# Performance work log

Hardware: AMD Instinct MI355X
Metric: run time of the kernel (lower is better)

## Reference

```python
import jax, jax.numpy as jnp
import numpy as np

L, P, R, A, V, B = 2, 3, 512, 196, 9487, 256


def setup_inputs() -> dict:
    key = jax.random.key(0)
    ks = jax.random.split(key, 20)
    s = 0.02
    inp = {
        "x": jax.random.normal(ks[0], (B, R), jnp.float32),
        "att": jax.random.normal(ks[1], (B, A, R), jnp.float32),
        "inputs": jax.random.normal(ks[2], (2 * L, B, R), jnp.float32),
        # per-layer, per-parallel LSTM core weights (torch Linear: y = x W^T + b)
        "i2h_w": s * jax.random.normal(ks[3], (L, P, 4 * R, R), jnp.float32),
        "i2h_b": s * jax.random.normal(ks[4], (L, P, 4 * R), jnp.float32),
        "h2h_w": s * jax.random.normal(ks[5], (L, P, 4 * R, R), jnp.float32),
        "h2h_b": s * jax.random.normal(ks[6], (L, P, 4 * R), jnp.float32),
        "a2h_w": s * jax.random.normal(ks[7], (L, P, 4 * R, R), jnp.float32),
        "a2h_b": s * jax.random.normal(ks[8], (L, P, 4 * R), jnp.float32),
        # 2 attention modules per layer
        "a2a_w": s * jax.random.normal(ks[9], (L, 2, A, R), jnp.float32),
        "a2a_b": s * jax.random.normal(ks[10], (L, 2, A), jnp.float32),
        "h2a_w": s * jax.random.normal(ks[11], (L, 2, A, R), jnp.float32),
        "h2a_b": s * jax.random.normal(ks[12], (L, 2, A), jnp.float32),
        "d2d_w": s * jax.random.normal(ks[13], (L, 2, A), jnp.float32),
        "d2d_b": s * jax.random.normal(ks[14], (L, 2), jnp.float32),
        "proj_w": s * jax.random.normal(ks[15], (V, R), jnp.float32),
        "proj_b": s * jax.random.normal(ks[16], (V,), jnp.float32),
    }
    return inp


def _soft_att(att, h, a2a_w, a2a_b, h2a_w, h2a_b, d2d_w, d2d_b):
    # att: [B,A,R], h: [B,R]
    v = jnp.einsum('bar,kr->bak', att, a2a_w) + a2a_b          # [B,A,A]
    hh = h @ h2a_w.T + h2a_b                                   # [B,A]
    dot = jnp.tanh(v + hh[:, :, None])                         # [B,A,A]
    score = jnp.einsum('bak,k->ba', dot, d2d_w) + d2d_b        # [B,A]
    w = jax.nn.softmax(score, axis=-1)
    return jnp.einsum('bar,ba->br', att, w)                    # [B,R]


def reference(x, att, inputs, i2h_w, i2h_b, h2h_w, h2h_b, a2h_w, a2h_b,
              a2a_w, a2a_b, h2a_w, h2a_b, d2d_w, d2d_b, proj_w, proj_b):
    outputs = []
    top_h = None
    for i in range(L):
        prev_c = inputs[2 * i]
        prev_h = inputs[2 * i + 1]
        xt = x if i == 0 else x + outputs[-1]
        att_res0 = _soft_att(att, prev_h, a2a_w[i, 0], a2a_b[i, 0],
                             h2a_w[i, 0], h2a_b[i, 0], d2d_w[i, 0], d2d_b[i, 0])
        # fused gates over the P parallel cores: [P,B,4R]
        sums = (jnp.einsum('bi,pgi->pbg', xt, i2h_w[i]) + i2h_b[i][:, None, :]
                + jnp.einsum('bi,pgi->pbg', prev_h, h2h_w[i]) + h2h_b[i][:, None, :]
                + jnp.einsum('bi,pgi->pbg', att_res0, a2h_w[i]) + a2h_b[i][:, None, :])
        sig = jax.nn.sigmoid(sums[..., :3 * R])
        in_g, fg_g, out_g = sig[..., :R], sig[..., R:2 * R], sig[..., 2 * R:3 * R]
        in_t = jnp.tanh(sums[..., 3 * R:])
        nc_p = fg_g * prev_c + in_g * in_t                     # [P,B,R]
        nh_p = out_g * jnp.tanh(nc_p)                          # [P,B,R]
        next_c = nc_p.mean(0)
        next_h = nh_p.mean(0)
        att_res1 = _soft_att(att, next_h, a2a_w[i, 1], a2a_b[i, 1],
                             h2a_w[i, 1], h2a_b[i, 1], d2d_w[i, 1], d2d_b[i, 1])
        top_h = att_res1 + next_h
        outputs.append(next_c)
        outputs.append(top_h)
    logsoft = jax.nn.log_softmax(top_h @ proj_w.T + proj_b, axis=-1)
    return jnp.stack(outputs), logsoft
```

## Files before the change

### kernel.cpp

```cpp
#include <hip/hip_runtime.h>
#include <hip/hip_bf16.h>
#include <math.h>

#define L_ 2
#define P_ 3
#define R_ 512
#define A_ 196
#define V_ 9487
#define B_ 256
#define BR (B_*R_)
#define G4 (4*R_)

typedef short bf16x8 __attribute__((ext_vector_type(8)));
typedef float f32x4  __attribute__((ext_vector_type(4)));

static __device__ __forceinline__ unsigned short f2b(float f){
  unsigned int u = __builtin_bit_cast(unsigned int, f);
  u += 0x7fffu + ((u >> 16) & 1u);
  return (unsigned short)(u >> 16);
}
static __device__ __forceinline__ bf16x8 cvt8(float4 a, float4 b){
  bf16x8 r;
  r[0]=(short)f2b(a.x); r[1]=(short)f2b(a.y); r[2]=(short)f2b(a.z); r[3]=(short)f2b(a.w);
  r[4]=(short)f2b(b.x); r[5]=(short)f2b(b.y); r[6]=(short)f2b(b.z); r[7]=(short)f2b(b.w);
  return r;
}

__global__ __launch_bounds__(256) void k_cvt(const float* __restrict__ src,
                                             short* __restrict__ dst, int n)
{
  const int c = blockIdx.x * 256 + threadIdx.x;
  const int base = c * 8;
  if (base >= n) return;
  float4 a = *(const float4*)(src + base);
  float4 b = *(const float4*)(src + base + 4);
  *(bf16x8*)(dst + base) = cvt8(a, b);
}

__global__ __launch_bounds__(256) void k_hh(
    const float* __restrict__ h, const float* __restrict__ hw,
    const float* __restrict__ hb, float* __restrict__ out)
{
  __shared__ float hred[64][5];
  const int t = threadIdx.x;
  const int row = blockIdx.x * 64 + (t >> 2);
  const int seg = t & 3;
  const int b = row / A_;
  const int a = row - b * A_;
  const float* hp = h  + (size_t)b * R_ + seg * 128;
  const float* wp = hw + (size_t)a * R_ + seg * 128;
  float p = 0.f;
#pragma unroll
  for (int k = 0; k < 128; k += 4) {
    float4 a4 = *(const float4*)(hp + k);
    float4 b4 = *(const float4*)(wp + k);
    p = fmaf(a4.x, b4.x, p); p = fmaf(a4.y, b4.y, p);
    p = fmaf(a4.z, b4.z, p); p = fmaf(a4.w, b4.w, p);
  }
  hred[t >> 2][seg] = p;
  __syncthreads();
  if (t < 64) {
    const int m = blockIdx.x * 64 + t;
    const int b2 = m / A_;
    const int a2 = m - b2 * A_;
    out[m] = hred[t][0] + hred[t][1] + hred[t][2] + hred[t][3] + hb[a2];
  }
}

__global__ __launch_bounds__(256) void k_score_mfma(
    const float* __restrict__ att, const short* __restrict__ wbf,
    const float* __restrict__ a2ab, const float* __restrict__ d2dw,
    const float* __restrict__ d2db, const float* __restrict__ hh,
    float* __restrict__ score)
{
  __shared__ __align__(16) short As[4 * 64 * 8];
  __shared__ __align__(16) short Bs[4 * 224 * 8];
  __shared__ float wpad[224], bpad[224], hhs[64], sred[2][64];

  const int t   = threadIdx.x;
  const int m0  = blockIdx.x * 64;
  const int wid = t >> 6, l = t & 63;
  const int wr  = wid >> 1, wc = wid & 1;
  const int q   = l >> 4, lc = l & 15;

  if (t < 224) { wpad[t] = (t < A_) ? d2dw[t] : 0.f; bpad[t] = (t < A_) ? a2ab[t] : 0.f; }
  if (t < 64)  hhs[t] = hh[m0 + t];

  f32x4 acc[2][7];
#pragma unroll
  for (int i = 0; i < 2; ++i)
#pragma unroll
    for (int j = 0; j < 7; ++j) acc[i][j] = (f32x4){0.f, 0.f, 0.f, 0.f};

  const int s_row = t >> 2, s_kb = t & 3;
  const float* asrc = att + (size_t)(m0 + s_row) * R_ + s_kb * 8;
  const int n3 = 192 + s_row;

  float4 ra0, ra1;
  bf16x8 rb0, rb1, rb2, rb3;

#define SC_LOAD(ks) {                                                   \
    const int k0 = (ks) * 32;                                           \
    ra0 = *(const float4*)(asrc + k0);                                  \
    ra1 = *(const float4*)(asrc + k0 + 4);                              \
    const int koff = k0 + s_kb * 8;                                     \
    rb0 = *(const bf16x8*)(wbf + (size_t)(s_row      ) * R_ + koff);    \
    rb1 = *(const bf16x8*)(wbf + (size_t)(s_row +  64) * R_ + koff);    \
    rb2 = *(const bf16x8*)(wbf + (size_t)(s_row + 128) * R_ + koff);    \
    if (t < 128) {                                                      \
      if (n3 < A_) rb3 = *(const bf16x8*)(wbf + (size_t)n3 * R_ + koff);\
      else         rb3 = (bf16x8){0,0,0,0,0,0,0,0};                     \
    }                                                                   \
  }
#define SC_STORE() {                                                    \
    *(bf16x8*)&As[s_kb * 512  + s_row * 8] = cvt8(ra0, ra1);            \
    *(bf16x8*)&Bs[s_kb * 1792 + (s_row      ) * 8] = rb0;               \
    *(bf16x8*)&Bs[s_kb * 1792 + (s_row +  64) * 8] = rb1;               \
    *(bf16x8*)&Bs[s_kb * 1792 + (s_row + 128) * 8] = rb2;               \
    if (t < 128) *(bf16x8*)&Bs[s_kb * 1792 + n3 * 8] = rb3;             \
  }

  SC_LOAD(0);
  for (int ks = 0; ks < 16; ++ks) {
    __syncthreads();
    SC_STORE();
    __syncthreads();
    if (ks < 15) SC_LOAD(ks + 1);
    bf16x8 af[2], bfr[7];
#pragma unroll
    for (int mf = 0; mf < 2; ++mf) {
      const int row = wr * 32 + mf * 16 + lc;
      af[mf] = *(const bf16x8*)&As[q * 512 + row * 8];
    }
#pragma unroll
    for (int nf = 0; nf < 7; ++nf) {
      const int n = wc * 112 + nf * 16 + lc;
      bfr[nf] = *(const bf16x8*)&Bs[q * 1792 + n * 8];
    }
#pragma unroll
    for (int mf = 0; mf < 2; ++mf)
#pragma unroll
      for (int nf = 0; nf < 7; ++nf)
        acc[mf][nf] = __builtin_amdgcn_mfma_f32_16x16x32_bf16(af[mf], bfr[nf], acc[mf][nf], 0, 0, 0);
  }
#undef SC_LOAD
#undef SC_STORE

  float s[2][4];
#pragma unroll
  for (int mf = 0; mf < 2; ++mf)
#pragma unroll
    for (int r = 0; r < 4; ++r) s[mf][r] = 0.f;

#pragma unroll
  for (int mf = 0; mf < 2; ++mf) {
    const int rbase = wr * 32 + mf * 16 + q * 4;
#pragma unroll
    for (int nf = 0; nf < 7; ++nf) {
      const int col = wc * 112 + nf * 16 + lc;
      const float bp = bpad[col], wp = wpad[col];
#pragma unroll
      for (int r = 0; r < 4; ++r)
        s[mf][r] += tanhf(acc[mf][nf][r] + bp + hhs[rbase + r]) * wp;
    }
  }
#pragma unroll
  for (int mask = 1; mask <= 8; mask <<= 1) {
#pragma unroll
    for (int mf = 0; mf < 2; ++mf)
#pragma unroll
      for (int r = 0; r < 4; ++r) s[mf][r] += __shfl_xor(s[mf][r], mask);
  }
  if (lc == 0) {
#pragma unroll
    for (int mf = 0; mf < 2; ++mf)
#pragma unroll
      for (int r = 0; r < 4; ++r)
        sred[wc][wr * 32 + mf * 16 + q * 4 + r] = s[mf][r];
  }
  __syncthreads();
  if (t < 64) score[m0 + t] = sred[0][t] + sred[1][t] + d2db[0];
}

__global__ __launch_bounds__(256) void k_softmax_att(float* __restrict__ sc)
{
  __shared__ float red[256];
  const int b = blockIdx.x, t = threadIdx.x;
  float v = (t < A_) ? sc[b*A_ + t] : -INFINITY;
  red[t] = v; __syncthreads();
  for (int s = 128; s > 0; s >>= 1) { if (t < s) red[t] = fmaxf(red[t], red[t+s]); __syncthreads(); }
  const float mx = red[0]; __syncthreads();
  const float e = (t < A_) ? expf(v - mx) : 0.f;
  red[t] = e; __syncthreads();
  for (int s = 128; s > 0; s >>= 1) { if (t < s) red[t] += red[t+s]; __syncthreads(); }
  if (t < A_) sc[b*A_ + t] = e / red[0];
}

__global__ __launch_bounds__(256) void k_attres(
    const float* __restrict__ att, const float* __restrict__ w, float* __restrict__ out)
{
  __shared__ float wl[A_];
  const int b = blockIdx.x, t = threadIdx.x;
  if (t < A_) wl[t] = w[b*A_ + t];
  __syncthreads();
  const int r = blockIdx.y * 256 + t;
  const float* ap = att + (size_t)b * A_ * R_ + r;
  float acc = 0.f;
#pragma unroll 4
  for (int a = 0; a < A_; ++a) acc = fmaf(ap[(size_t)a * R_], wl[a], acc);
  out[b * R_ + r] = acc;
}

__global__ __launch_bounds__(256) void k_lstm_mfma(
    const float* __restrict__ xt, const float* __restrict__ ph, const float* __restrict__ ar,
    const short* __restrict__ wi, const short* __restrict__ wh, const short* __restrict__ wa,
    int layer, float* __restrict__ sums)
{
  __shared__ __align__(16) short As[4 * 64 * 8];
  __shared__ __align__(16) short Bs[4 * 128 * 8];

  const int t   = threadIdx.x;
  const int m0  = blockIdx.x * 64;
  const int n0  = blockIdx.y * 128;
  const int wid = t >> 6, l = t & 63;
  const int wr  = wid >> 1, wc = wid & 1;
  const int q   = l >> 4, lc = l & 15;

  f32x4 acc[2][4];
#pragma unroll
  for (int i = 0; i < 2; ++i)
#pragma unroll
    for (int j = 0; j < 4; ++j) acc[i][j] = (f32x4){0.f, 0.f, 0.f, 0.f};

  const int s_row = t >> 2, s_kb = t & 3;
  const size_t wrow0 = ((size_t)layer * 6144 + n0) * R_;

  float4 ra0, ra1;
  bf16x8 rb0, rb1;

#define LS_LOAD(ks) {                                                   \
    const int seg = (ks) >> 4;                                          \
    const int kk  = ((ks) & 15) * 32;                                   \
    const float* asel = (seg == 0) ? xt : (seg == 1) ? ph : ar;         \
    const float* ap = asel + (size_t)(m0 + s_row) * R_ + kk + s_kb * 8; \
    ra0 = *(const float4*)ap;                                           \
    ra1 = *(const float4*)(ap + 4);                                     \
    const short* wsel = (seg == 0) ? wi : (seg == 1) ? wh : wa;         \
    const short* bp0 = wsel + wrow0 + (size_t)(s_row      ) * R_ + kk + s_kb * 8; \
    const short* bp1 = wsel + wrow0 + (size_t)(s_row +  64) * R_ + kk + s_kb * 8; \
    rb0 = *(const bf16x8*)bp0;                                          \
    rb1 = *(const bf16x8*)bp1;                                          \
  }
#define LS_STORE() {                                                    \
    *(bf16x8*)&As[s_kb * 512  + s_row * 8] = cvt8(ra0, ra1);            \
    *(bf16x8*)&Bs[s_kb * 1024 + (s_row      ) * 8] = rb0;               \
    *(bf16x8*)&Bs[s_kb * 1024 + (s_row + 64) * 8] = rb1;                \
  }

  LS_LOAD(0);
  for (int ks = 0; ks < 48; ++ks) {
    __syncthreads();
    LS_STORE();
    __syncthreads();
    if (ks < 47) LS_LOAD(ks + 1);
    bf16x8 af[2], bfr[4];
#pragma unroll
    for (int mf = 0; mf < 2; ++mf) {
      const int row = wr * 32 + mf * 16 + lc;
      af[mf] = *(const bf16x8*)&As[q * 512 + row * 8];
    }
#pragma unroll
    for (int nf = 0; nf < 4; ++nf) {
      const int n = wc * 64 + nf * 16 + lc;
      bfr[nf] = *(const bf16x8*)&Bs[q * 1024 + n * 8];
    }
#pragma unroll
    for (int mf = 0; mf < 2; ++mf)
#pragma unroll
      for (int nf = 0; nf < 4; ++nf)
        acc[mf][nf] = __builtin_amdgcn_mfma_f32_16x16x32_bf16(af[mf], bfr[nf], acc[mf][nf], 0, 0, 0);
  }
#undef LS_LOAD
#undef LS_STORE

#pragma unroll
  for (int mf = 0; mf < 2; ++mf) {
#pragma unroll
    for (int nf = 0; nf < 4; ++nf) {
      const int col = n0 + wc * 64 + nf * 16 + lc;
      const int p = col >> 11, g = col & 2047;
#pragma unroll
      for (int r = 0; r < 4; ++r) {
        const int b = m0 + wr * 32 + mf * 16 + q * 4 + r;
        sums[((size_t)p * B_ + b) * (size_t)G4 + g] = acc[mf][nf][r];
      }
    }
  }
}

__global__ __launch_bounds__(256) void k_lstm_elem(
    const float* __restrict__ sums,
    const float* __restrict__ i2hb, const float* __restrict__ h2hb, const float* __restrict__ a2hb,
    const float* __restrict__ prev_c, int layer,
    float* __restrict__ out_c, float* __restrict__ next_h)
{
  const int idx = blockIdx.x * 256 + threadIdx.x;
  const int b = idx >> 9, r = idx & 511;
  const size_t boff = (size_t)layer * P_ * G4;
  const float pc = prev_c[idx];
  float aC = 0.f, aH = 0.f;
#pragma unroll
  for (int p = 0; p < P_; ++p) {
    const float* sp = sums + ((size_t)p * B_ + b) * (size_t)G4;
    const float* b1 = i2hb + boff + p * G4;
    const float* b2 = h2hb + boff + p * G4;
    const float* b3 = a2hb + boff + p * G4;
    const float gi = sp[r]      + b1[r]      + b2[r]      + b3[r];
    const float gf = sp[r+512]  + b1[r+512]  + b2[r+512]  + b3[r+512];
    const float go = sp[r+1024] + b1[r+1024] + b2[r+1024] + b3[r+1024];
    const float gt = sp[r+1536] + b1[r+1536] + b2[r+1536] + b3[r+1536];
    const float ig = 1.f / (1.f + expf(-gi));
    const float fg = 1.f / (1.f + expf(-gf));
    const float og = 1.f / (1.f + expf(-go));
    const float it = tanhf(gt);
    const float nc = fg * pc + ig * it;
    const float nh = og * tanhf(nc);
    aC += nc; aH += nh;
  }
  out_c[idx]  = aC * (1.f/3.f);
  next_h[idx] = aH * (1.f/3.f);
}

__global__ __launch_bounds__(256) void k_toph(
    const float* __restrict__ attres, const float* __restrict__ nh, const float* __restrict__ x,
    float* __restrict__ out_slot, float* __restrict__ toph, float* __restrict__ xt_next, int make_xt)
{
  const int idx = blockIdx.x * 256 + threadIdx.x;
  const float v = attres[idx] + nh[idx];
  out_slot[idx] = v;
  toph[idx] = v;
  if (make_xt) xt_next[idx] = x[idx] + v;
}

__global__ __launch_bounds__(256) void k_proj_mfma(
    const float* __restrict__ th, const short* __restrict__ pwb,
    const float* __restrict__ pb, float* __restrict__ logits)
{
  __shared__ __align__(16) short As[4 * 64 * 8];
  __shared__ __align__(16) short Bs[4 * 128 * 8];

  const int t   = threadIdx.x;
  const int m0  = blockIdx.x * 64;
  const int n0  = blockIdx.y * 128;
  const int wid = t >> 6, l = t & 63;
  const int wr  = wid >> 1, wc = wid & 1;
  const int q   = l >> 4, lc = l & 15;

  f32x4 acc[2][4];
#pragma unroll
  for (int i = 0; i < 2; ++i)
#pragma unroll
    for (int j = 0; j < 4; ++j) acc[i][j] = (f32x4){0.f, 0.f, 0.f, 0.f};

  const int s_row = t >> 2, s_kb = t & 3;
  const int ng0 = n0 + s_row, ng1 = n0 + s_row + 64;

  float4 ra0, ra1;
  bf16x8 rb0, rb1;

#define PJ_LOAD(ks) {                                                   \
    const int kk = (ks) * 32;                                           \
    const float* ap = th + (size_t)(m0 + s_row) * R_ + kk + s_kb * 8;   \
    ra0 = *(const float4*)ap;                                           \
    ra1 = *(const float4*)(ap + 4);                                     \
    if (ng0 < V_) rb0 = *(const bf16x8*)(pwb + (size_t)ng0 * R_ + kk + s_kb * 8); \
    else          rb0 = (bf16x8){0,0,0,0,0,0,0,0};                      \
    if (ng1 < V_) rb1 = *(const bf16x8*)(pwb + (size_t)ng1 * R_ + kk + s_kb * 8); \
    else          rb1 = (bf16x8){0,0,0,0,0,0,0,0};                      \
  }
#define PJ_STORE() {                                                    \
    *(bf16x8*)&As[s_kb * 512  + s_row * 8] = cvt8(ra0, ra1);            \
    *(bf16x8*)&Bs[s_kb * 1024 + (s_row      ) * 8] = rb0;               \
    *(bf16x8*)&Bs[s_kb * 1024 + (s_row + 64) * 8] = rb1;                \
  }

  PJ_LOAD(0);
  for (int ks = 0; ks < 16; ++ks) {
    __syncthreads();
    PJ_STORE();
    __syncthreads();
    if (ks < 15) PJ_LOAD(ks + 1);
    bf16x8 af[2], bfr[4];
#pragma unroll
    for (int mf = 0; mf < 2; ++mf) {
      const int row = wr * 32 + mf * 16 + lc;
      af[mf] = *(const bf16x8*)&As[q * 512 + row * 8];
    }
#pragma unroll
    for (int nf = 0; nf < 4; ++nf) {
      const int n = wc * 64 + nf * 16 + lc;
      bfr[nf] = *(const bf16x8*)&Bs[q * 1024 + n * 8];
    }
#pragma unroll
    for (int mf = 0; mf < 2; ++mf)
#pragma unroll
      for (int nf = 0; nf < 4; ++nf)
        acc[mf][nf] = __builtin_amdgcn_mfma_f32_16x16x32_bf16(af[mf], bfr[nf], acc[mf][nf], 0, 0, 0);
  }
#undef PJ_LOAD
#undef PJ_STORE

#pragma unroll
  for (int mf = 0; mf < 2; ++mf) {
#pragma unroll
    for (int nf = 0; nf < 4; ++nf) {
      const int col = n0 + wc * 64 + nf * 16 + lc;
      if (col < V_) {
        const float bias = pb[col];
#pragma unroll
        for (int r = 0; r < 4; ++r) {
          const int b = m0 + wr * 32 + mf * 16 + q * 4 + r;
          logits[(size_t)b * V_ + col] = acc[mf][nf][r] + bias;
        }
      }
    }
  }
}

__global__ __launch_bounds__(256) void k_logsoftmax(
    const float* __restrict__ logits, float* __restrict__ out)
{
  __shared__ float red[256];
  const int b = blockIdx.x, t = threadIdx.x;
  const float* lp = logits + (size_t)b * V_;
  float mx = -INFINITY;
  for (int n = t; n < V_; n += 256) mx = fmaxf(mx, lp[n]);
  red[t] = mx; __syncthreads();
  for (int s = 128; s > 0; s >>= 1) { if (t < s) red[t] = fmaxf(red[t], red[t+s]); __syncthreads(); }
  mx = red[0]; __syncthreads();
  float sm = 0.f;
  for (int n = t; n < V_; n += 256) sm += expf(lp[n] - mx);
  red[t] = sm; __syncthreads();
  for (int s = 128; s > 0; s >>= 1) { if (t < s) red[t] += red[t+s]; __syncthreads(); }
  const float lse = mx + logf(red[0]);
  float* op = out + (size_t)b * V_;
  for (int n = t; n < V_; n += 256) op[n] = lp[n] - lse;
}

extern "C" void kernel_launch(void* const* d_in, const int* in_sizes, int n_in,
                              void* d_out, int out_size, void* d_ws, size_t ws_size,
                              hipStream_t stream)
{
  const float* x      = (const float*)d_in[0];
  const float* att    = (const float*)d_in[1];
  const float* inputs = (const float*)d_in[2];
  const float* i2hw   = (const float*)d_in[3];
  const float* i2hb   = (const float*)d_in[4];
  const float* h2hw   = (const float*)d_in[5];
  const float* h2hb   = (const float*)d_in[6];
  const float* a2hw   = (const float*)d_in[7];
  const float* a2hb   = (const float*)d_in[8];
  const float* a2aw   = (const float*)d_in[9];
  const float* a2ab   = (const float*)d_in[10];
  const float* h2aw   = (const float*)d_in[11];
  const float* h2ab   = (const float*)d_in[12];
  const float* d2dw   = (const float*)d_in[13];
  const float* d2db   = (const float*)d_in[14];
  const float* pw     = (const float*)d_in[15];
  const float* pb     = (const float*)d_in[16];
  float* out = (float*)d_out;
  float* ws  = (float*)d_ws;

  float* w_score  = ws + 0;
  float* w_hh     = ws + 51200;
  float* w_attres = ws + 102400;
  float* w_xt     = ws + 233472;
  float* w_nexth  = ws + 364544;
  float* w_toph   = ws + 495616;
  float* w_sums   = ws + 626688;
  float* w_logits = ws + 2199552;

  short* bfbase = (short*)(ws + 4628480);
  short* aw_bf  = bfbase;
  short* wi_bf  = bfbase + 401408;
  short* wh_bf  = bfbase + 6692864;
  short* wa_bf  = bfbase + 12984320;
  short* pw_bf  = bfbase + 19275776;

  k_cvt<<<196,  256, 0, stream>>>(a2aw, aw_bf, 401408);
  k_cvt<<<3072, 256, 0, stream>>>(i2hw, wi_bf, 6291456);
  k_cvt<<<3072, 256, 0, stream>>>(h2hw, wh_bf, 6291456);
  k_cvt<<<3072, 256, 0, stream>>>(a2hw, wa_bf, 6291456);
  k_cvt<<<2372, 256, 0, stream>>>(pw,   pw_bf, 4857344);

  const float* cur_x = x;
  for (int i = 0; i < L_; ++i) {
    const float* prev_c = inputs + (size_t)(2*i)   * BR;
    const float* prev_h = inputs + (size_t)(2*i+1) * BR;

    {
      const int idx = i*2 + 0;
      k_hh<<<784, 256, 0, stream>>>(prev_h, h2aw + (size_t)idx*A_*R_, h2ab + (size_t)idx*A_, w_hh);
      k_score_mfma<<<784, 256, 0, stream>>>(att, aw_bf + (size_t)idx*A_*R_,
          a2ab + (size_t)idx*A_, d2dw + (size_t)idx*A_, d2db + idx, w_hh, w_score);
      k_softmax_att<<<B_, 256, 0, stream>>>(w_score);
      k_attres<<<dim3(B_, 2), 256, 0, stream>>>(att, w_score, w_attres);
    }

    k_lstm_mfma<<<dim3(4, 48), 256, 0, stream>>>(cur_x, prev_h, w_attres,
                                                 wi_bf, wh_bf, wa_bf, i, w_sums);
    k_lstm_elem<<<512, 256, 0, stream>>>(w_sums, i2hb, h2hb, a2hb, prev_c, i,
                                         out + (size_t)(2*i) * BR, w_nexth);

    {
      const int idx = i*2 + 1;
      k_hh<<<784, 256, 0, stream>>>(w_nexth, h2aw + (size_t)idx*A_*R_, h2ab + (size_t)idx*A_, w_hh);
      k_score_mfma<<<784, 256, 0, stream>>>(att, aw_bf + (size_t)idx*A_*R_,
          a2ab + (size_t)idx*A_, d2dw + (size_t)idx*A_, d2db + idx, w_hh, w_score);
      k_softmax_att<<<B_, 256, 0, stream>>>(w_score);
      k_attres<<<dim3(B_, 2), 256, 0, stream>>>(att, w_score, w_attres);
    }

    k_toph<<<512, 256, 0, stream>>>(w_attres, w_nexth, x,
                                    out + (size_t)(2*i+1) * BR, w_toph, w_xt,
                                    (i == 0) ? 1 : 0);
    cur_x = w_xt;
  }

  k_proj_mfma<<<dim3(4, 75), 256, 0, stream>>>(w_toph, pw_bf, pb, w_logits);
  k_logsoftmax<<<B_, 256, 0, stream>>>(w_logits, out + (size_t)4 * BR);
}
```

Measured before the change: 752.0 us.

## Convert att to bf16 once, use async LDS loads and fuse softmax with attres

Adds a one-time pass that converts the whole att tensor to bf16 and pads the a2a weights to 256 rows. The score GEMM then loads tiles straight into LDS with global_load_lds, using a swizzled, double-buffered layout, instead of converting float att inside each tile. Softmax and the attention-weighted sum are merged into one kernel that reads bf16 att, which halves the bytes read per attention pass. The cost is an extra conversion pass over the 25.7M-element att tensor (read 103MB fp32, write 51MB bf16) and lower precision in attres.

```diff
diff --git a/kernel.cpp b/kernel.cpp
--- a/kernel.cpp
+++ b/kernel.cpp
@@ -13,11 +13,16 @@
 
 typedef short bf16x8 __attribute__((ext_vector_type(8)));
 typedef float f32x4  __attribute__((ext_vector_type(4)));
+typedef unsigned int u32;
 
 static __device__ __forceinline__ unsigned short f2b(float f){
-  unsigned int u = __builtin_bit_cast(unsigned int, f);
+  u32 u = __builtin_bit_cast(u32, f);
   u += 0x7fffu + ((u >> 16) & 1u);
   return (unsigned short)(u >> 16);
+}
+static __device__ __forceinline__ float b2f(short s){
+  u32 u = ((u32)(unsigned short)s) << 16;
+  return __builtin_bit_cast(float, u);
 }
 static __device__ __forceinline__ bf16x8 cvt8(float4 a, float4 b){
   bf16x8 r;
@@ -25,6 +30,14 @@
   r[4]=(short)f2b(b.x); r[5]=(short)f2b(b.y); r[6]=(short)f2b(b.z); r[7]=(short)f2b(b.w);
   return r;
 }
+
+static __device__ __forceinline__ void gld16(const void* g, void* l){
+  __builtin_amdgcn_global_load_lds(
+      (const __attribute__((address_space(1))) u32*)g,
+      (__attribute__((address_space(3))) u32*)l, 16, 0, 0);
+}
+
+#define SW(x) ((((x)&3) ^ (((x)>>2)&3)))
 
 __global__ __launch_bounds__(256) void k_cvt(const float* __restrict__ src,
                                              short* __restrict__ dst, int n)
@@ -35,6 +48,24 @@
   float4 a = *(const float4*)(src + base);
   float4 b = *(const float4*)(src + base + 4);
   *(bf16x8*)(dst + base) = cvt8(a, b);
+}
+
+__global__ __launch_bounds__(256) void k_cvt_pad_aw(const float* __restrict__ src,
+                                                    short* __restrict__ dst)
+{
+  const int idx8 = (blockIdx.x * 256 + threadIdx.x) * 8;
+  const int g   = idx8 >> 17;
+  const int rem = idx8 & 131071;
+  const int row = rem >> 9;
+  const int k   = rem & 511;
+  bf16x8 v;
+  if (row < A_) {
+    const float* sp = src + ((size_t)g * A_ + row) * R_ + k;
+    v = cvt8(*(const float4*)sp, *(const float4*)(sp + 4));
+  } else {
+    v = (bf16x8){0,0,0,0,0,0,0,0};
+  }
+  *(bf16x8*)(dst + idx8) = v;
 }
 
 __global__ __launch_bounds__(256) void k_hh(
@@ -68,14 +99,14 @@
 }
 
 __global__ __launch_bounds__(256) void k_score_mfma(
-    const float* __restrict__ att, const short* __restrict__ wbf,
+    const short* __restrict__ att_bf, const short* __restrict__ wbf,
     const float* __restrict__ a2ab, const float* __restrict__ d2dw,
     const float* __restrict__ d2db, const float* __restrict__ hh,
     float* __restrict__ score)
 {
-  __shared__ __align__(16) short As[4 * 64 * 8];
-  __shared__ __align__(16) short Bs[4 * 224 * 8];
-  __shared__ float wpad[224], bpad[224], hhs[64], sred[2][64];
+  __shared__ __align__(16) short As[2][256 * 8];
+  __shared__ __align__(16) short Bs[2][1024 * 8];
+  __shared__ float wpad[256], bpad[256], hhs[64], sred[2][64];
 
   const int t   = threadIdx.x;
   const int m0  = blockIdx.x * 64;
@@ -83,68 +114,59 @@
   const int wr  = wid >> 1, wc = wid & 1;
   const int q   = l >> 4, lc = l & 15;
 
-  if (t < 224) { wpad[t] = (t < A_) ? d2dw[t] : 0.f; bpad[t] = (t < A_) ? a2ab[t] : 0.f; }
-  if (t < 64)  hhs[t] = hh[m0 + t];
-
-  f32x4 acc[2][7];
+  wpad[t] = (t < A_) ? d2dw[t] : 0.f;
+  bpad[t] = (t < A_) ? a2ab[t] : 0.f;
+  if (t < 64) hhs[t] = hh[m0 + t];
+
+  f32x4 acc[2][8];
 #pragma unroll
   for (int i = 0; i < 2; ++i)
 #pragma unroll
-    for (int j = 0; j < 7; ++j) acc[i][j] = (f32x4){0.f, 0.f, 0.f, 0.f};
-
-  const int s_row = t >> 2, s_kb = t & 3;
-  const float* asrc = att + (size_t)(m0 + s_row) * R_ + s_kb * 8;
-  const int n3 = 192 + s_row;
-
-  float4 ra0, ra1;
-  bf16x8 rb0, rb1, rb2, rb3;
-
-#define SC_LOAD(ks) {                                                   \
-    const int k0 = (ks) * 32;                                           \
-    ra0 = *(const float4*)(asrc + k0);                                  \
-    ra1 = *(const float4*)(asrc + k0 + 4);                              \
-    const int koff = k0 + s_kb * 8;                                     \
-    rb0 = *(const bf16x8*)(wbf + (size_t)(s_row      ) * R_ + koff);    \
-    rb1 = *(const bf16x8*)(wbf + (size_t)(s_row +  64) * R_ + koff);    \
-    rb2 = *(const bf16x8*)(wbf + (size_t)(s_row + 128) * R_ + koff);    \
-    if (t < 128) {                                                      \
-      if (n3 < A_) rb3 = *(const bf16x8*)(wbf + (size_t)n3 * R_ + koff);\
-      else         rb3 = (bf16x8){0,0,0,0,0,0,0,0};                     \
-    }                                                                   \
-  }
-#define SC_STORE() {                                                    \
-    *(bf16x8*)&As[s_kb * 512  + s_row * 8] = cvt8(ra0, ra1);            \
-    *(bf16x8*)&Bs[s_kb * 1792 + (s_row      ) * 8] = rb0;               \
-    *(bf16x8*)&Bs[s_kb * 1792 + (s_row +  64) * 8] = rb1;               \
-    *(bf16x8*)&Bs[s_kb * 1792 + (s_row + 128) * 8] = rb2;               \
-    if (t < 128) *(bf16x8*)&Bs[s_kb * 1792 + n3 * 8] = rb3;             \
-  }
-
-  SC_LOAD(0);
+    for (int j = 0; j < 8; ++j) acc[i][j] = (f32x4){0.f, 0.f, 0.f, 0.f};
+
+  const int a_row  = t >> 2;
+  const int a_kb   = (t & 3) ^ SW(a_row);
+  const short* a_g = att_bf + (size_t)(m0 + a_row) * R_ + a_kb * 8;
+  int b_n[4], b_kb[4];
+#pragma unroll
+  for (int j = 0; j < 4; ++j) {
+    b_n[j]  = j * 64 + (t >> 2);
+    b_kb[j] = (t & 3) ^ SW(b_n[j]);
+  }
+
+#define STAGE(bufi, kz) {                                                 \
+    gld16((const void*)(a_g + (kz)), (void*)&As[bufi][wid * 512]);        \
+    _Pragma("unroll")                                                     \
+    for (int j = 0; j < 4; ++j)                                           \
+      gld16((const void*)(wbf + (size_t)b_n[j] * R_ + (kz) + b_kb[j] * 8),\
+            (void*)&Bs[bufi][j * 2048 + wid * 512]);                      \
+  }
+
+  STAGE(0, 0);
+  __syncthreads();
+
   for (int ks = 0; ks < 16; ++ks) {
-    __syncthreads();
-    SC_STORE();
-    __syncthreads();
-    if (ks < 15) SC_LOAD(ks + 1);
-    bf16x8 af[2], bfr[7];
+    const int cur = ks & 1;
+    if (ks < 15) STAGE(cur ^ 1, (ks + 1) * 32);
+    bf16x8 af[2], bfr[8];
 #pragma unroll
     for (int mf = 0; mf < 2; ++mf) {
       const int row = wr * 32 + mf * 16 + lc;
-      af[mf] = *(const bf16x8*)&As[q * 512 + row * 8];
-    }
-#pragma unroll
-    for (int nf = 0; nf < 7; ++nf) {
-      const int n = wc * 112 + nf * 16 + lc;
-      bfr[nf] = *(const bf16x8*)&Bs[q * 1792 + n * 8];
+      af[mf] = *(const bf16x8*)&As[cur][(row * 4 + (q ^ SW(row))) * 8];
+    }
+#pragma unroll
+    for (int nf = 0; nf < 8; ++nf) {
+      const int n = wc * 128 + nf * 16 + lc;
+      bfr[nf] = *(const bf16x8*)&Bs[cur][(n * 4 + (q ^ SW(n))) * 8];
     }
 #pragma unroll
     for (int mf = 0; mf < 2; ++mf)
 #pragma unroll
-      for (int nf = 0; nf < 7; ++nf)
+      for (int nf = 0; nf < 8; ++nf)
         acc[mf][nf] = __builtin_amdgcn_mfma_f32_16x16x32_bf16(af[mf], bfr[nf], acc[mf][nf], 0, 0, 0);
-  }
-#undef SC_LOAD
-#undef SC_STORE
+    __syncthreads();
+  }
+#undef STAGE
 
   float s[2][4];
 #pragma unroll
@@ -156,8 +178,8 @@
   for (int mf = 0; mf < 2; ++mf) {
     const int rbase = wr * 32 + mf * 16 + q * 4;
 #pragma unroll
-    for (int nf = 0; nf < 7; ++nf) {
-      const int col = wc * 112 + nf * 16 + lc;
+    for (int nf = 0; nf < 8; ++nf) {
+      const int col = wc * 128 + nf * 16 + lc;
       const float bp = bpad[col], wp = wpad[col];
 #pragma unroll
       for (int r = 0; r < 4; ++r)
@@ -182,32 +204,29 @@
   if (t < 64) score[m0 + t] = sred[0][t] + sred[1][t] + d2db[0];
 }
 
-__global__ __launch_bounds__(256) void k_softmax_att(float* __restrict__ sc)
+__global__ __launch_bounds__(256) void k_smax_attres(
+    const float* __restrict__ sc, const short* __restrict__ att_bf,
+    float* __restrict__ out)
 {
   __shared__ float red[256];
+  __shared__ float wl[256];
   const int b = blockIdx.x, t = threadIdx.x;
-  float v = (t < A_) ? sc[b*A_ + t] : -INFINITY;
+  const float v = (t < A_) ? sc[b * A_ + t] : -INFINITY;
   red[t] = v; __syncthreads();
   for (int s = 128; s > 0; s >>= 1) { if (t < s) red[t] = fmaxf(red[t], red[t+s]); __syncthreads(); }
   const float mx = red[0]; __syncthreads();
   const float e = (t < A_) ? expf(v - mx) : 0.f;
   red[t] = e; __syncthreads();
   for (int s = 128; s > 0; s >>= 1) { if (t < s) red[t] += red[t+s]; __syncthreads(); }
-  if (t < A_) sc[b*A_ + t] = e / red[0];
-}
-
-__global__ __launch_bounds__(256) void k_attres(
-    const float* __restrict__ att, const float* __restrict__ w, float* __restrict__ out)
-{
-  __shared__ float wl[A_];
-  const int b = blockIdx.x, t = threadIdx.x;
-  if (t < A_) wl[t] = w[b*A_ + t];
+  wl[t] = e / red[0];
   __syncthreads();
+
   const int r = blockIdx.y * 256 + t;
-  const float* ap = att + (size_t)b * A_ * R_ + r;
+  const short* ap = att_bf + (size_t)b * A_ * R_ + r;
   float acc = 0.f;
+  int a = 0;
 #pragma unroll 4
-  for (int a = 0; a < A_; ++a) acc = fmaf(ap[(size_t)a * R_], wl[a], acc);
+  for (; a < 196; ++a) acc = fmaf(b2f(ap[(size_t)a * R_]), wl[a], acc);
   out[b * R_ + r] = acc;
 }
 
@@ -481,13 +500,15 @@
   float* w_logits = ws + 2199552;
 
   short* bfbase = (short*)(ws + 4628480);
-  short* aw_bf  = bfbase;
-  short* wi_bf  = bfbase + 401408;
-  short* wh_bf  = bfbase + 6692864;
-  short* wa_bf  = bfbase + 12984320;
-  short* pw_bf  = bfbase + 19275776;
-
-  k_cvt<<<196,  256, 0, stream>>>(a2aw, aw_bf, 401408);
+  short* att_bf = bfbase;
+  short* awp_bf = bfbase + 25690112;
+  short* wi_bf  = bfbase + 26214400;
+  short* wh_bf  = bfbase + 32505856;
+  short* wa_bf  = bfbase + 38797312;
+  short* pw_bf  = bfbase + 45088768;
+
+  k_cvt<<<12544, 256, 0, stream>>>(att, att_bf, 25690112);
+  k_cvt_pad_aw<<<256, 256, 0, stream>>>(a2aw, awp_bf);
   k_cvt<<<3072, 256, 0, stream>>>(i2hw, wi_bf, 6291456);
   k_cvt<<<3072, 256, 0, stream>>>(h2hw, wh_bf, 6291456);
   k_cvt<<<3072, 256, 0, stream>>>(a2hw, wa_bf, 6291456);
@@ -501,10 +522,9 @@
     {
       const int idx = i*2 + 0;
       k_hh<<<784, 256, 0, stream>>>(prev_h, h2aw + (size_t)idx*A_*R_, h2ab + (size_t)idx*A_, w_hh);
-      k_score_mfma<<<784, 256, 0, stream>>>(att, aw_bf + (size_t)idx*A_*R_,
+      k_score_mfma<<<784, 256, 0, stream>>>(att_bf, awp_bf + (size_t)idx*256*R_,
           a2ab + (size_t)idx*A_, d2dw + (size_t)idx*A_, d2db + idx, w_hh, w_score);
-      k_softmax_att<<<B_, 256, 0, stream>>>(w_score);
-      k_attres<<<dim3(B_, 2), 256, 0, stream>>>(att, w_score, w_attres);
+      k_smax_attres<<<dim3(B_, 2), 256, 0, stream>>>(w_score, att_bf, w_attres);
     }
 
     k_lstm_mfma<<<dim3(4, 48), 256, 0, stream>>>(cur_x, prev_h, w_attres,
@@ -515,10 +535,9 @@
     {
       const int idx = i*2 + 1;
       k_hh<<<784, 256, 0, stream>>>(w_nexth, h2aw + (size_t)idx*A_*R_, h2ab + (size_t)idx*A_, w_hh);
-      k_score_mfma<<<784, 256, 0, stream>>>(att, aw_bf + (size_t)idx*A_*R_,
+      k_score_mfma<<<784, 256, 0, stream>>>(att_bf, awp_bf + (size_t)idx*256*R_,
           a2ab + (size_t)idx*A_, d2dw + (size_t)idx*A_, d2db + idx, w_hh, w_score);
-      k_softmax_att<<<B_, 256, 0, stream>>>(w_score);
-      k_attres<<<dim3(B_, 2), 256, 0, stream>>>(att, w_score, w_attres);
+      k_smax_attres<<<dim3(B_, 2), 256, 0, stream>>>(w_score, att_bf, w_attres);
     }
 
     k_toph<<<512, 256, 0, stream>>>(w_attres, w_nexth, x,
```

After: 747.0 us. No clear change (-0.7%).
